# Optimization experiments

Hardware: AMD Instinct MI355X
Metric: run time of the kernel (lower is better)

## Reference

```python
import jax, jax.numpy as jnp
import numpy as np

N_NODES = 50000
N_EDGES = 800000
HEADS = 6
LEAKY = 0.2


def gat_layer(x, W, a_src, a_dst, src, dst):
    """Multi-head GAT layer (Velickovic et al.), concat heads + ELU.
    x: [N, F_in], W: [H, F_in, F_out], a_src/a_dst: [H, F_out]."""
    n = x.shape[0]
    h = jnp.einsum('nf,hfo->nho', x, W)              # [N, H, F_out]
    es = jnp.einsum('nho,ho->nh', h, a_src)          # source attention term
    ed = jnp.einsum('nho,ho->nh', h, a_dst)          # destination attention term
    e = jax.nn.leaky_relu(es[src] + ed[dst], LEAKY)  # [E, H] per-edge logits
    # segment softmax over incoming edges of each destination node
    emax = jax.ops.segment_max(e, dst, num_segments=n)
    emax = jnp.where(jnp.isfinite(emax), emax, jnp.zeros_like(emax))
    ex = jnp.exp(e - emax[dst])                      # [E, H]
    denom = jax.ops.segment_sum(ex, dst, num_segments=n)
    alpha = ex / (denom[dst] + 1e-16)                # [E, H]
    msg = alpha[:, :, None] * h[src]                 # [E, H, F_out]
    out = jax.ops.segment_sum(msg, dst, num_segments=n)  # [N, H, F_out]
    return jax.nn.elu(out).reshape(n, -1)            # concat heads


def setup_inputs() -> dict:
    key = jax.random.key(0)
    ks = jax.random.split(key, 16)
    glorot = lambda k, shape: jax.random.normal(k, shape, jnp.float32) * np.sqrt(2.0 / (shape[-2] + shape[-1]))
    inp = {
        'x': jax.random.normal(ks[0], (N_NODES, 11), jnp.float32),
        'edge_index': jax.random.randint(ks[1], (2, N_EDGES), 0, N_NODES, jnp.int32),
        'W1': glorot(ks[2], (HEADS, 11, 16)),
        'a1s': glorot(ks[3], (HEADS, 16)),
        'a1d': glorot(ks[4], (HEADS, 16)),
        'W2': glorot(ks[5], (HEADS, 96, 32)),
        'a2s': glorot(ks[6], (HEADS, 32)),
        'a2d': glorot(ks[7], (HEADS, 32)),
        'W3': glorot(ks[8], (HEADS, 192, 64)),
        'a3s': glorot(ks[9], (HEADS, 64)),
        'a3d': glorot(ks[10], (HEADS, 64)),
        'Wd': glorot(ks[11], (384, 1)),
        'bd': jnp.zeros((1,), jnp.float32),
    }
    return inp


def reference(x, edge_index, W1, a1s, a1d, W2, a2s, a2d, W3, a3s, a3d, Wd, bd):
    src, dst = edge_index[0], edge_index[1]
    h = gat_layer(x, W1, a1s, a1d, src, dst)   # [N, 96]
    h = gat_layer(h, W2, a2s, a2d, src, dst)   # [N, 192]
    h = gat_layer(h, W3, a3s, a3d, src, dst)   # [N, 384]
    g = jnp.sum(h, axis=0).reshape(1, -1)      # sum pool -> [1, 384]
    g = g / jnp.maximum(jnp.linalg.norm(g, axis=1, keepdims=True), 1e-12)  # F.normalize
    out = g @ Wd + bd                          # Dense 384->1, linear nonlin
    return jnp.squeeze(out, 1)                 # [1]
```

## Files before the change

### kernel.cpp

```cpp
#include <hip/hip_runtime.h>
#include <hip/hip_bf16.h>


#define HHEADS 6

typedef __attribute__((ext_vector_type(8))) short bf16x8;
typedef __attribute__((ext_vector_type(4))) float f32x4;
typedef __attribute__((ext_vector_type(2))) float f32x2;

typedef __attribute__((address_space(3))) unsigned int lds_uint;
typedef const __attribute__((address_space(1))) unsigned int glb_uint;

__device__ __forceinline__ float bfl(unsigned u) { return __uint_as_float(u << 16); }
__device__ __forceinline__ float bfh(unsigned u) { return __uint_as_float(u & 0xffff0000u); }
__device__ __forceinline__ unsigned short f2bf(float v) {
    unsigned u = __float_as_uint(v);
    return (unsigned short)((u + 0x7fffu + ((u >> 16) & 1u)) >> 16);
}
__device__ __forceinline__ float bf2f(unsigned short h) {
    return __uint_as_float((unsigned)h << 16);
}
__device__ __forceinline__ unsigned fkey(float f) {
    unsigned u = __float_as_uint(f);
    return (u >> 31) ? ~u : (u | 0x80000000u);
}
__device__ __forceinline__ float funkey(unsigned k) {
    return (k >> 31) ? __uint_as_float(k & 0x7fffffffu) : __uint_as_float(~k);
}

__device__ __forceinline__ void xpose4(float& v0, float& v1, float& v2, float& v3, int b) {
    bool hi = (b & 2) != 0;
    float s0 = hi ? v0 : v2;
    float s1 = hi ? v1 : v3;
    s0 = __shfl_xor(s0, 2, 64);
    s1 = __shfl_xor(s1, 2, 64);
    v0 = hi ? s0 : v0;
    v1 = hi ? s1 : v1;
    v2 = hi ? v2 : s0;
    v3 = hi ? v3 : s1;
    bool od = (b & 1) != 0;
    float t0 = od ? v0 : v1;
    t0 = __shfl_xor(t0, 1, 64);
    v0 = od ? t0 : v0;
    v1 = od ? v1 : t0;
    float t1 = od ? v2 : v3;
    t1 = __shfl_xor(t1, 1, 64);
    v2 = od ? t1 : v2;
    v3 = od ? v3 : t1;
}

__global__ void zero_misc(int* __restrict__ count, int* __restrict__ cursor,
                          float* __restrict__ g, unsigned* __restrict__ gmax,
                          unsigned short* __restrict__ apH,
                          long pad3_off, long pad3_cnt, long pad6_off, long pad6_cnt, int n) {
    long i = (long)blockIdx.x * blockDim.x + threadIdx.x;
    long stride = (long)gridDim.x * blockDim.x;
    for (long j = i; j < n; j += stride) {
        count[j] = 0;
        cursor[j] = 0;
    }
    if (i < 384) g[i] = 0.f;
    if (i < 12) gmax[i] = 0u;
    for (long j = i; j < pad3_cnt; j += stride) apH[pad3_off + j] = 0;
    for (long j = i; j < pad6_cnt; j += stride) apH[pad6_off + j] = 0;
}

__global__ void hist_kernel(const int* __restrict__ dst, int* __restrict__ count, int E) {
    int e = blockIdx.x * blockDim.x + threadIdx.x;
    if (e >= E) return;
    atomicAdd(&count[dst[e]], 1);
}

__global__ void scan_block(const int* __restrict__ count, int* __restrict__ offsets,
                           int* __restrict__ bsum, int n) {
    __shared__ int s[1024];
    int i = blockIdx.x * 1024 + threadIdx.x;
    int v = (i < n) ? count[i] : 0;
    s[threadIdx.x] = v;
    __syncthreads();
    for (int off = 1; off < 1024; off <<= 1) {
        int t = (threadIdx.x >= (unsigned)off) ? s[threadIdx.x - off] : 0;
        __syncthreads();
        s[threadIdx.x] += t;
        __syncthreads();
    }
    if (i < n) offsets[i] = s[threadIdx.x] - v;
    if (threadIdx.x == 1023) bsum[blockIdx.x] = s[1023];
}

__global__ void scan_tops(int* __restrict__ bsum, int nb) {
    __shared__ int s[64];
    int t = threadIdx.x;
    int v = (t < nb) ? bsum[t] : 0;
    s[t] = v;
    __syncthreads();
    for (int off = 1; off < 64; off <<= 1) {
        int tmp = (t >= off) ? s[t - off] : 0;
        __syncthreads();
        s[t] += tmp;
        __syncthreads();
    }
    if (t < nb) bsum[t] = s[t] - v;
}

__global__ void scan_add(int* __restrict__ offsets, const int* __restrict__ bsum, int n,
                         int total) {
    int i = blockIdx.x * 1024 + threadIdx.x;
    if (i < n) offsets[i] += bsum[blockIdx.x];
    if (i == 0) offsets[n] = total;
}

__global__ void scatter_kernel(const int* __restrict__ src, const int* __restrict__ dst,
                               const int* __restrict__ offsets, int* __restrict__ cursor,
                               int* __restrict__ ssrc, int E) {
    int e = blockIdx.x * blockDim.x + threadIdx.x;
    if (e >= E) return;
    int d = dst[e];
    int pos = offsets[d] + atomicAdd(&cursor[d], 1);
    ssrc[pos] = src[e];
}

__global__ void repack_w(const float* __restrict__ W, float* __restrict__ Wp, int FIN, int F) {
    int HF = HHEADS * F;
    int i = blockIdx.x * blockDim.x + threadIdx.x;
    if (i >= FIN * HF) return;
    int k = i / HF, c = i % HF;
    int hd = c / F, f = c % F;
    Wp[i] = W[(hd * FIN + k) * F + f];
}

__global__ void repack_w_mfma(const float* __restrict__ W, unsigned short* __restrict__ bh,
                              int FIN, int F, int NPAD) {
    int i = blockIdx.x * blockDim.x + threadIdx.x;
    if (i >= FIN * NPAD) return;
    int k = i / NPAD, n = i % NPAD;
    int NKT = FIN / 32;
    int HF = HHEADS * F;
    float w = 0.f;
    if (n < HF) {
        int hd = n / F, f = n % F;
        w = W[(hd * FIN + k) * F + f];
    }
    size_t e = ((size_t)((n >> 4) * NKT + (k >> 5)) * 64 + ((n & 15) | (((k >> 3) & 3) << 4))) * 8 +
               (k & 7);
    bh[e] = f2bf(w);
}

template <int BM, int BN, int BK>
__global__ __launch_bounds__(256) void gemm_small_attn(const float* __restrict__ A,
                                                       const float* __restrict__ B,
                                                       unsigned char* __restrict__ C8,
                                                       const float* __restrict__ as_,
                                                       const float* __restrict__ ad_,
                                                       float* __restrict__ es,
                                                       float* __restrict__ ed, int M, int K,
                                                       int N) {
    __shared__ float As[BK][BM + 4];
    __shared__ float Bs[BK][BN];
    int tid = threadIdx.x;
    int tx = tid % 16, ty = tid / 16;
    int m0 = blockIdx.y * BM, n0 = blockIdx.x * BN;
    float acc[4][4] = {};
    for (int kk0 = 0; kk0 < K; kk0 += BK) {
#pragma unroll
        for (int i = 0; i < (BM * BK) / 256; ++i) {
            int idx = tid + i * 256;
            int m = idx / BK, k = idx % BK;
            float v = 0.f;
            if (m0 + m < M && kk0 + k < K) v = A[(size_t)(m0 + m) * K + kk0 + k];
            As[k][m] = v;
        }
#pragma unroll
        for (int i = 0; i < (BK * BN) / 1024; ++i) {
            int idx = tid + i * 256;
            int k = idx / (BN / 4), n4 = idx % (BN / 4);
            float4 v = make_float4(0.f, 0.f, 0.f, 0.f);
            if (kk0 + k < K && n0 + n4 * 4 < N)
                v = *(const float4*)&B[(size_t)(kk0 + k) * N + n0 + n4 * 4];
            *(float4*)&Bs[k][n4 * 4] = v;
        }
        __syncthreads();
#pragma unroll
        for (int k = 0; k < BK; ++k) {
            float4 av = *(const float4*)&As[k][ty * 4];
            float4 bv = *(const float4*)&Bs[k][tx * 4];
            float a[4] = {av.x, av.y, av.z, av.w};
            float b[4] = {bv.x, bv.y, bv.z, bv.w};
#pragma unroll
            for (int i = 0; i < 4; ++i)
#pragma unroll
                for (int j = 0; j < 4; ++j) acc[i][j] += a[i] * b[j];
        }
        __syncthreads();
    }
    bool colok = (n0 + tx * 4) < N;
    float asv[4], adv[4];
#pragma unroll
    for (int j = 0; j < 4; ++j) {
        int col = n0 + tx * 4 + j;
        asv[j] = (col < N) ? as_[col] : 0.f;
        adv[j] = (col < N) ? ad_[col] : 0.f;
    }
#pragma unroll
    for (int i = 0; i < 4; ++i) {
        int m = m0 + ty * 4 + i;
        bool mok = m < M;
        if (mok && colok) {
            int pk = __builtin_amdgcn_cvt_pk_fp8_f32(acc[i][0], acc[i][1], 0, false);
            pk = __builtin_amdgcn_cvt_pk_fp8_f32(acc[i][2], acc[i][3], pk, true);
            *(unsigned*)&C8[(size_t)m * N + n0 + tx * 4] = (unsigned)pk;
        }
        float ps = 0.f, pd = 0.f;
#pragma unroll
        for (int j = 0; j < 4; ++j) {
            ps += acc[i][j] * asv[j];
            pd += acc[i][j] * adv[j];
        }
        ps += __shfl_down(ps, 2, 4);
        ps += __shfl_down(ps, 1, 4);
        pd += __shfl_down(pd, 2, 4);
        pd += __shfl_down(pd, 1, 4);
        if (mok && colok && (tx & 3) == 0) {
            int hd = (n0 + tx * 4) >> 4;
            es[(size_t)m * HHEADS + hd] = ps;
            ed[(size_t)m * HHEADS + hd] = pd;
        }
    }
}

template <int K, int NREAL, int NPAD, int F, int MT>
__global__ __launch_bounds__(256) void gemm_attn_mfma(
    const unsigned short* __restrict__ Ah, const unsigned short* __restrict__ Bh,
    unsigned char* __restrict__ C8, const float* __restrict__ as_,
    const float* __restrict__ ad_, float* __restrict__ es, float* __restrict__ ed,
    unsigned* __restrict__ gmax, int M) {
    constexpr int NKT = K / 32;
    __shared__ unsigned short sB[NKT * 4096];
    __shared__ unsigned short sA[2][4096];
    int tid = threadIdx.x;
    int lane = tid & 63, wave = tid >> 6;
    int wrow = wave >> 1, wcol = wave & 1;
    int quad = lane >> 4, c16 = lane & 15;

    int nwg = gridDim.x * gridDim.y;
    int hh = blockIdx.y * gridDim.x + blockIdx.x;
    int q = nwg >> 3, r = nwg & 7;
    int xcd = hh & 7, pos = hh >> 3;
    int wk = (xcd < r ? xcd * (q + 1) : r * (q + 1) + (xcd - r) * q) + pos;
    int bx = wk % gridDim.x, by = wk / gridDim.x;

    int n0 = bx * 128;
    int bn16 = n0 >> 4;
    int nmt = (M + 127) >> 7;

#pragma unroll
    for (int kt2 = 0; kt2 < NKT; ++kt2) {
#pragma unroll
        for (int rep = 0; rep < 2; ++rep) {
            int chunk = tid + rep * 256;
            int tile = chunk >> 6, e8 = chunk & 63;
            size_t boff = ((size_t)((bn16 + tile) * NKT + kt2) * 64 + e8) * 8;
            __builtin_amdgcn_global_load_lds((glb_uint*)&Bh[boff],
                                             (lds_uint*)&sB[kt2 * 4096 + chunk * 8], 16, 0, 0);
        }
    }
    auto STAGE_A = [&](int mti, int kt2, int buf) {
#pragma unroll
        for (int rep = 0; rep < 2; ++rep) {
            int chunk = tid + rep * 256;
            int tile = chunk >> 6, e8 = chunk & 63;
            size_t aoff = ((size_t)((mti * 8 + tile) * NKT + kt2) * 64 + e8) * 8;
            __builtin_amdgcn_global_load_lds((glb_uint*)&Ah[aoff],
                                             (lds_uint*)&sA[buf][chunk * 8], 16, 0, 0);
        }
    };
    STAGE_A(min(by * MT, nmt - 1), 0, 0);
    asm volatile("s_waitcnt vmcnt(0)" ::: "memory");
    __builtin_amdgcn_s_barrier();

    float asv[4], adv[4];
#pragma unroll
    for (int j = 0; j < 4; ++j) {
        int col = n0 + wcol * 64 + j * 16 + c16;
        bool ok = col < NREAL;
        asv[j] = ok ? as_[col] : 0.f;
        adv[j] = ok ? ad_[col] : 0.f;
    }
    float mx = -1e30f;
    float mxA = -1e30f, mxB = -1e30f;
    bool colvalid = (n0 + wcol * 64) < NREAL;
    int b4 = lane & 3;

    f32x4 acc[4][4] = {};
    const int T = MT * NKT;
    int mt = 0, kt = 0;
    for (int t = 0; t < T; ++t) {
        int cur = t & 1;
        int nkt = kt + 1, nmt2 = mt;
        if (nkt == NKT) {
            nkt = 0;
            nmt2 = mt + 1;
        }
        if (t + 1 < T) STAGE_A(min(by * MT + nmt2, nmt - 1), nkt, cur ^ 1);
        bf16x8 fah[4], fbh[4];
#pragma unroll
        for (int i = 0; i < 4; ++i) {
            fah[i] = *(const bf16x8*)&sA[cur][(wrow * 4 + i) * 512 + lane * 8];
            fbh[i] = *(const bf16x8*)&sB[kt * 4096 + (wcol * 4 + i) * 512 + lane * 8];
        }
        asm volatile("s_waitcnt lgkmcnt(0)" ::: "memory");
        __builtin_amdgcn_sched_barrier(0);
#pragma unroll
        for (int i = 0; i < 4; ++i)
#pragma unroll
            for (int j = 0; j < 4; ++j)
                acc[i][j] = __builtin_amdgcn_mfma_f32_16x16x32_bf16(fah[i], fbh[j], acc[i][j],
                                                                    0, 0, 0);
        if (kt == NKT - 1) {
            int m0 = (by * MT + mt) * 128;
            if (m0 < M) {
#pragma unroll
                for (int i = 0; i < 4; ++i) {
#pragma unroll
                    for (int r2 = 0; r2 < 4; ++r2) {
                        int m = m0 + wrow * 64 + i * 16 + quad * 4 + r2;
                        bool mok = m < M;
                        if (F == 64) {
                            float ps = acc[i][0][r2] * asv[0] + acc[i][1][r2] * asv[1] +
                                       acc[i][2][r2] * asv[2] + acc[i][3][r2] * asv[3];
                            float pd = acc[i][0][r2] * adv[0] + acc[i][1][r2] * adv[1] +
                                       acc[i][2][r2] * adv[2] + acc[i][3][r2] * adv[3];
#pragma unroll
                            for (int off = 8; off > 0; off >>= 1) {
                                ps += __shfl_down(ps, off, 16);
                                pd += __shfl_down(pd, off, 16);
                            }
                            if (mok && c16 == 0) {
                                int hd = (n0 + wcol * 64) / 64;
                                es[(size_t)m * HHEADS + hd] = ps;
                                ed[(size_t)m * HHEADS + hd] = pd;
                                mx = fmaxf(mx, ps);
                            }
                        } else {
                            float psA = acc[i][0][r2] * asv[0] + acc[i][1][r2] * asv[1];
                            float pdA = acc[i][0][r2] * adv[0] + acc[i][1][r2] * adv[1];
                            float psB = acc[i][2][r2] * asv[2] + acc[i][3][r2] * asv[3];
                            float pdB = acc[i][2][r2] * adv[2] + acc[i][3][r2] * adv[3];
#pragma unroll
                            for (int off = 8; off > 0; off >>= 1) {
                                psA += __shfl_down(psA, off, 16);
                                pdA += __shfl_down(pdA, off, 16);
                                psB += __shfl_down(psB, off, 16);
                                pdB += __shfl_down(pdB, off, 16);
                            }
                            if (mok && c16 == 0 && colvalid) {
                                int colbase = n0 + wcol * 64;
                                int hd = colbase / 32;
                                es[(size_t)m * HHEADS + hd] = psA;
                                ed[(size_t)m * HHEADS + hd] = pdA;
                                es[(size_t)m * HHEADS + hd + 1] = psB;
                                ed[(size_t)m * HHEADS + hd + 1] = pdB;
                                mxA = fmaxf(mxA, psA);
                                mxB = fmaxf(mxB, psB);
                            }
                        }
                    }
                }
#pragma unroll
                for (int i = 0; i < 4; ++i) {
                    int m = m0 + wrow * 64 + i * 16 + quad * 4 + b4;
                    bool mok = m < M;
#pragma unroll
                    for (int j = 0; j < 4; ++j) {
                        float v0 = acc[i][j][0], v1 = acc[i][j][1], v2 = acc[i][j][2],
                              v3 = acc[i][j][3];
                        xpose4(v0, v1, v2, v3, b4);
                        int colb = n0 + wcol * 64 + j * 16 + (c16 & 12);
                        if (mok && (F == 64 || colvalid)) {
                            int pk = __builtin_amdgcn_cvt_pk_fp8_f32(v0, v1, 0, false);
                            pk = __builtin_amdgcn_cvt_pk_fp8_f32(v2, v3, pk, true);
                            *(unsigned*)&C8[(size_t)m * NREAL + colb] = (unsigned)pk;
                        }
                    }
                }
            }
#pragma unroll
            for (int i = 0; i < 4; ++i)
#pragma unroll
                for (int j = 0; j < 4; ++j) acc[i][j] = (f32x4){0.f, 0.f, 0.f, 0.f};
        }
        asm volatile("s_waitcnt vmcnt(0)" ::: "memory");
        __builtin_amdgcn_s_barrier();
        kt = nkt;
        mt = nmt2;
    }

    if (F == 64) {
#pragma unroll
        for (int off = 32; off > 0; off >>= 1) mx = fmaxf(mx, __shfl_xor(mx, off));
        if (lane == 0) atomicMax(&gmax[(n0 + wcol * 64) / 64], fkey(mx));
    } else {
        mxA = fmaxf(mxA, __shfl_xor(mxA, 16));
        mxA = fmaxf(mxA, __shfl_xor(mxA, 32));
        mxB = fmaxf(mxB, __shfl_xor(mxB, 16));
        mxB = fmaxf(mxB, __shfl_xor(mxB, 32));
        if (lane == 0 && colvalid) {
            int hd = (n0 + wcol * 64) / 32;
            atomicMax(&gmax[6 + hd], fkey(mxA));
            atomicMax(&gmax[6 + hd + 1], fkey(mxB));
        }
    }
}

template <int F>
__global__ __launch_bounds__(256) void aggregate_fused(
    const unsigned char* __restrict__ h8, const float* __restrict__ es,
    const float* __restrict__ ed, const int* __restrict__ offsets,
    const int* __restrict__ ssrc, unsigned short* __restrict__ oh, int n) {
    constexpr int HF = HHEADS * F;
    constexpr int C8 = HF / 8;
    int tid = blockIdx.x * blockDim.x + threadIdx.x;
    if (tid >= n * C8) return;
    int node = tid / C8, q = tid % C8;
    int c = q * 8, hd = c / F;
    int a = offsets[node], b = offsets[node + 1];
    float edv = ed[node * HHEADS + hd];
    float m = -1e30f, l = 0.f;
    f32x2 a0 = {0.f, 0.f}, a1 = {0.f, 0.f}, a2 = {0.f, 0.f}, a3 = {0.f, 0.f};
    for (int j = a; j < b; ++j) {
        int s = ssrc[j];
        float v = es[s * HHEADS + hd] + edv;
        v = v > 0.f ? v : 0.2f * v;
        float mn = fmaxf(m, v);
        float r = __expf(m - mn);
        float wgt = __expf(v - mn);
        uint2 hv = *(const uint2*)&h8[(size_t)s * HF + c];
        f32x2 p0 = __builtin_amdgcn_cvt_pk_f32_fp8((int)hv.x, false);
        f32x2 p1 = __builtin_amdgcn_cvt_pk_f32_fp8((int)hv.x, true);
        f32x2 p2 = __builtin_amdgcn_cvt_pk_f32_fp8((int)hv.y, false);
        f32x2 p3 = __builtin_amdgcn_cvt_pk_f32_fp8((int)hv.y, true);
        l = l * r + wgt;
        f32x2 rv = {r, r}, wv = {wgt, wgt};
        a0 = a0 * rv + wv * p0;
        a1 = a1 * rv + wv * p1;
        a2 = a2 * rv + wv * p2;
        a3 = a3 * rv + wv * p3;
        m = mn;
    }
    float invd = 1.0f / (l + 1e-16f);
    float res[8] = {a0[0], a0[1], a1[0], a1[1], a2[0], a2[1], a3[0], a3[1]};
    unsigned short th[8];
#pragma unroll
    for (int k = 0; k < 8; ++k) {
        float v = res[k] * invd;
        v = v > 0.f ? v : (__expf(v) - 1.0f);
        th[k] = f2bf(v);
    }
    constexpr int NKT = HF / 32;
    int lq = (node & 15) | (((c >> 3) & 3) << 4);
    size_t base = ((size_t)((node >> 4) * NKT + (c >> 5)) * 64 + lq) * 8;
    *(uint4*)&oh[base] = *(uint4*)th;
}

__global__ __launch_bounds__(256) void aggregate_wpn2(
    const unsigned char* __restrict__ h8, const float* __restrict__ es,
    const float* __restrict__ ed, const unsigned* __restrict__ gmax,
    const int* __restrict__ offsets, const int* __restrict__ ssrc,
    unsigned short* __restrict__ oh, int n) {
    constexpr int HF = 192;
    int wid = (int)((blockIdx.x * (unsigned)blockDim.x + threadIdx.x) >> 6);
    int lane = threadIdx.x & 63;
    if (wid >= n || lane >= 48) return;
    int node = wid;
    int hd = lane >> 3;
    int c = lane * 4;
    int a = offsets[node], b = offsets[node + 1];
    float edv = ed[node * HHEADS + hd];
    float mv = funkey(gmax[6 + hd]) + edv;
    float m = mv > 0.f ? mv : 0.2f * mv;
    float l = 0.f;
    f32x2 a0 = {0.f, 0.f}, a1 = {0.f, 0.f};
    const unsigned char* hbase = h8 + c;
    int j = a;
    for (; j + 3 < b; j += 4) {
        int s0 = ssrc[j], s1 = ssrc[j + 1], s2 = ssrc[j + 2], s3 = ssrc[j + 3];
        float ev0 = es[(size_t)s0 * HHEADS + hd];
        float ev1 = es[(size_t)s1 * HHEADS + hd];
        float ev2 = es[(size_t)s2 * HHEADS + hd];
        float ev3 = es[(size_t)s3 * HHEADS + hd];
        unsigned h0 = *(const unsigned*)(hbase + (size_t)s0 * HF);
        unsigned h1 = *(const unsigned*)(hbase + (size_t)s1 * HF);
        unsigned h2 = *(const unsigned*)(hbase + (size_t)s2 * HF);
        unsigned h3 = *(const unsigned*)(hbase + (size_t)s3 * HF);
        float v0 = ev0 + edv;
        v0 = v0 > 0.f ? v0 : 0.2f * v0;
        float v1 = ev1 + edv;
        v1 = v1 > 0.f ? v1 : 0.2f * v1;
        float v2 = ev2 + edv;
        v2 = v2 > 0.f ? v2 : 0.2f * v2;
        float v3 = ev3 + edv;
        v3 = v3 > 0.f ? v3 : 0.2f * v3;
        float w0 = __expf(v0 - m);
        float w1 = __expf(v1 - m);
        float w2 = __expf(v2 - m);
        float w3 = __expf(v3 - m);
        {
            f32x2 p0 = __builtin_amdgcn_cvt_pk_f32_fp8((int)h0, false);
            f32x2 p1 = __builtin_amdgcn_cvt_pk_f32_fp8((int)h0, true);
            f32x2 wv = {w0, w0};
            l += w0;
            a0 = a0 + wv * p0;
            a1 = a1 + wv * p1;
        }
        {
            f32x2 p0 = __builtin_amdgcn_cvt_pk_f32_fp8((int)h1, false);
            f32x2 p1 = __builtin_amdgcn_cvt_pk_f32_fp8((int)h1, true);
            f32x2 wv = {w1, w1};
            l += w1;
            a0 = a0 + wv * p0;
            a1 = a1 + wv * p1;
        }
        {
            f32x2 p0 = __builtin_amdgcn_cvt_pk_f32_fp8((int)h2, false);
            f32x2 p1 = __builtin_amdgcn_cvt_pk_f32_fp8((int)h2, true);
            f32x2 wv = {w2, w2};
            l += w2;
            a0 = a0 + wv * p0;
            a1 = a1 + wv * p1;
        }
        {
            f32x2 p0 = __builtin_amdgcn_cvt_pk_f32_fp8((int)h3, false);
            f32x2 p1 = __builtin_amdgcn_cvt_pk_f32_fp8((int)h3, true);
            f32x2 wv = {w3, w3};
            l += w3;
            a0 = a0 + wv * p0;
            a1 = a1 + wv * p1;
        }
    }
    for (; j < b; ++j) {
        int s0 = ssrc[j];
        float ev0 = es[(size_t)s0 * HHEADS + hd];
        unsigned h0 = *(const unsigned*)(hbase + (size_t)s0 * HF);
        float v0 = ev0 + edv;
        v0 = v0 > 0.f ? v0 : 0.2f * v0;
        float w0 = __expf(v0 - m);
        f32x2 p0 = __builtin_amdgcn_cvt_pk_f32_fp8((int)h0, false);
        f32x2 p1 = __builtin_amdgcn_cvt_pk_f32_fp8((int)h0, true);
        f32x2 wv = {w0, w0};
        l += w0;
        a0 = a0 + wv * p0;
        a1 = a1 + wv * p1;
    }
    float invd = 1.0f / (l + 1e-16f);
    float res[4] = {a0[0], a0[1], a1[0], a1[1]};
    unsigned short th[4];
#pragma unroll
    for (int k = 0; k < 4; ++k) {
        float v = res[k] * invd;
        v = v > 0.f ? v : (__expf(v) - 1.0f);
        th[k] = f2bf(v);
    }
    int lq = (node & 15) | (((c >> 3) & 3) << 4);
    size_t base = ((size_t)((node >> 4) * (HF / 32) + (c >> 5)) * 64 + lq) * 8 + (c & 7);
    *(uint2*)&oh[base] = *(uint2*)th;
}

__global__ __launch_bounds__(256) void aggregate_wpn3(
    const unsigned char* __restrict__ h8, const float* __restrict__ es,
    const float* __restrict__ ed, const unsigned* __restrict__ gmax,
    const int* __restrict__ offsets, const int* __restrict__ ssrc,
    __hip_bfloat16* __restrict__ outb, int n) {
    constexpr int HF = 384;
    int wid = (int)((blockIdx.x * (unsigned)blockDim.x + threadIdx.x) >> 6);
    int lane = threadIdx.x & 63;
    if (wid >= n || lane >= 48) return;
    int node = wid;
    int hd = lane >> 3;
    int c = lane * 8;
    int a = offsets[node], b = offsets[node + 1];
    float edv = ed[node * HHEADS + hd];
    float mv = funkey(gmax[hd]) + edv;
    float m = mv > 0.f ? mv : 0.2f * mv;
    float l = 0.f;
    f32x2 a0 = {0.f, 0.f}, a1 = {0.f, 0.f}, a2 = {0.f, 0.f}, a3 = {0.f, 0.f};
    const unsigned char* hbase = h8 + c;
    int j = a;
    for (; j + 3 < b; j += 4) {
        int s0 = ssrc[j], s1 = ssrc[j + 1], s2 = ssrc[j + 2], s3 = ssrc[j + 3];
        float ev0 = es[(size_t)s0 * HHEADS + hd];
        float ev1 = es[(size_t)s1 * HHEADS + hd];
        float ev2 = es[(size_t)s2 * HHEADS + hd];
        float ev3 = es[(size_t)s3 * HHEADS + hd];
        uint2 h0 = *(const uint2*)(hbase + (size_t)s0 * HF);
        uint2 h1 = *(const uint2*)(hbase + (size_t)s1 * HF);
        uint2 h2 = *(const uint2*)(hbase + (size_t)s2 * HF);
        uint2 h3 = *(const uint2*)(hbase + (size_t)s3 * HF);
        float v0 = ev0 + edv;
        v0 = v0 > 0.f ? v0 : 0.2f * v0;
        float v1 = ev1 + edv;
        v1 = v1 > 0.f ? v1 : 0.2f * v1;
        float v2 = ev2 + edv;
        v2 = v2 > 0.f ? v2 : 0.2f * v2;
        float v3 = ev3 + edv;
        v3 = v3 > 0.f ? v3 : 0.2f * v3;
        float w0 = __expf(v0 - m);
        float w1 = __expf(v1 - m);
        float w2 = __expf(v2 - m);
        float w3 = __expf(v3 - m);
        {
            f32x2 p0 = __builtin_amdgcn_cvt_pk_f32_fp8((int)h0.x, false);
            f32x2 p1 = __builtin_amdgcn_cvt_pk_f32_fp8((int)h0.x, true);
            f32x2 p2 = __builtin_amdgcn_cvt_pk_f32_fp8((int)h0.y, false);
            f32x2 p3 = __builtin_amdgcn_cvt_pk_f32_fp8((int)h0.y, true);
            f32x2 wv = {w0, w0};
            l += w0;
            a0 = a0 + wv * p0;
            a1 = a1 + wv * p1;
            a2 = a2 + wv * p2;
            a3 = a3 + wv * p3;
        }
        {
            f32x2 p0 = __builtin_amdgcn_cvt_pk_f32_fp8((int)h1.x, false);
            f32x2 p1 = __builtin_amdgcn_cvt_pk_f32_fp8((int)h1.x, true);
            f32x2 p2 = __builtin_amdgcn_cvt_pk_f32_fp8((int)h1.y, false);
            f32x2 p3 = __builtin_amdgcn_cvt_pk_f32_fp8((int)h1.y, true);
            f32x2 wv = {w1, w1};
            l += w1;
            a0 = a0 + wv * p0;
            a1 = a1 + wv * p1;
            a2 = a2 + wv * p2;
            a3 = a3 + wv * p3;
        }
        {
            f32x2 p0 = __builtin_amdgcn_cvt_pk_f32_fp8((int)h2.x, false);
            f32x2 p1 = __builtin_amdgcn_cvt_pk_f32_fp8((int)h2.x, true);
            f32x2 p2 = __builtin_amdgcn_cvt_pk_f32_fp8((int)h2.y, false);
            f32x2 p3 = __builtin_amdgcn_cvt_pk_f32_fp8((int)h2.y, true);
            f32x2 wv = {w2, w2};
            l += w2;
            a0 = a0 + wv * p0;
            a1 = a1 + wv * p1;
            a2 = a2 + wv * p2;
            a3 = a3 + wv * p3;
        }
        {
            f32x2 p0 = __builtin_amdgcn_cvt_pk_f32_fp8((int)h3.x, false);
            f32x2 p1 = __builtin_amdgcn_cvt_pk_f32_fp8((int)h3.x, true);
            f32x2 p2 = __builtin_amdgcn_cvt_pk_f32_fp8((int)h3.y, false);
            f32x2 p3 = __builtin_amdgcn_cvt_pk_f32_fp8((int)h3.y, true);
            f32x2 wv = {w3, w3};
            l += w3;
            a0 = a0 + wv * p0;
            a1 = a1 + wv * p1;
            a2 = a2 + wv * p2;
            a3 = a3 + wv * p3;
        }
    }
    for (; j < b; ++j) {
        int s0 = ssrc[j];
        float ev0 = es[(size_t)s0 * HHEADS + hd];
        uint2 h0 = *(const uint2*)(hbase + (size_t)s0 * HF);
        float v0 = ev0 + edv;
        v0 = v0 > 0.f ? v0 : 0.2f * v0;
        float w0 = __expf(v0 - m);
        f32x2 p0 = __builtin_amdgcn_cvt_pk_f32_fp8((int)h0.x, false);
        f32x2 p1 = __builtin_amdgcn_cvt_pk_f32_fp8((int)h0.x, true);
        f32x2 p2 = __builtin_amdgcn_cvt_pk_f32_fp8((int)h0.y, false);
        f32x2 p3 = __builtin_amdgcn_cvt_pk_f32_fp8((int)h0.y, true);
        f32x2 wv = {w0, w0};
        l += w0;
        a0 = a0 + wv * p0;
        a1 = a1 + wv * p1;
        a2 = a2 + wv * p2;
        a3 = a3 + wv * p3;
    }
    float invd = 1.0f / (l + 1e-16f);
    float res[8] = {a0[0], a0[1], a1[0], a1[1], a2[0], a2[1], a3[0], a3[1]};
    __hip_bfloat16 tb[8];
#pragma unroll
    for (int k = 0; k < 8; ++k) {
        float v = res[k] * invd;
        v = v > 0.f ? v : (__expf(v) - 1.0f);
        tb[k] = __float2bfloat16(v);
    }
    *(uint4*)&outb[(size_t)node * HF + c] = *(uint4*)tb;
}

__global__ void pool_kernel(const __hip_bfloat16* __restrict__ out3, float* __restrict__ g,
                            int n) {
    int b = blockIdx.x, t = threadIdx.x;
    int chunk = (n + gridDim.x - 1) / gridDim.x;
    int n0 = b * chunk, n1 = min(n, n0 + chunk);
    float a0 = 0.f, a1 = 0.f;
    const unsigned* p = (const unsigned*)out3;
    for (int node = n0; node < n1; ++node) {
        unsigned u = p[(size_t)node * 192 + t];
        a0 += bfl(u);
        a1 += bfh(u);
    }
    atomicAdd(&g[2 * t], a0);
    atomicAdd(&g[2 * t + 1], a1);
}

__global__ void final_kernel(const float* __restrict__ g, const float* __restrict__ Wd,
                             const float* __restrict__ bd, float* __restrict__ outp) {
    __shared__ float red[384];
    int t = threadIdx.x;
    float v = g[t];
    red[t] = v * v;
    __syncthreads();
    for (int s = 192; s >= 3; s >>= 1) {
        if (t < s) red[t] += red[t + s];
        __syncthreads();
    }
    __shared__ float scale_s;
    if (t == 0) {
        float norm = sqrtf(red[0] + red[1] + red[2]);
        scale_s = 1.0f / fmaxf(norm, 1e-12f);
    }
    __syncthreads();
    float scale = scale_s;
    red[t] = v * scale * Wd[t];
    __syncthreads();
    for (int s = 192; s >= 3; s >>= 1) {
        if (t < s) red[t] += red[t + s];
        __syncthreads();
    }
    if (t == 0) outp[0] = red[0] + red[1] + red[2] + bd[0];
}

extern "C" void kernel_launch(void* const* d_in, const int* in_sizes, int n_in, void* d_out,
                              int out_size, void* d_ws, size_t ws_size, hipStream_t stream) {
    const float* x = (const float*)d_in[0];
    const int* ei = (const int*)d_in[1];
    const float* W1 = (const float*)d_in[2];
    const float* a1s = (const float*)d_in[3];
    const float* a1d = (const float*)d_in[4];
    const float* W2 = (const float*)d_in[5];
    const float* a2s = (const float*)d_in[6];
    const float* a2d = (const float*)d_in[7];
    const float* W3 = (const float*)d_in[8];
    const float* a3s = (const float*)d_in[9];
    const float* a3d = (const float*)d_in[10];
    const float* Wd = (const float*)d_in[11];
    const float* bd = (const float*)d_in[12];
    float* outp = (float*)d_out;

    const int N = in_sizes[0] / 11;
    const int E = in_sizes[1] / 2;
    const int* src = ei;
    const int* dst = ei + E;

    const int NT16 = ((N + 127) / 128) * 8;
    const int NMT = (N + 127) / 128;

    char* w = (char*)d_ws;
    size_t off = 0;
    auto A = [&](size_t bytes) {
        size_t o = off;
        off += (bytes + 255) & ~(size_t)255;
        return o;
    };
    unsigned char* bufH = (unsigned char*)(w + A((size_t)N * 384 * 2));
    __hip_bfloat16* bufO = (__hip_bfloat16*)(w + A((size_t)N * 384 * 2));
    unsigned short* apH = (unsigned short*)(w + A((size_t)NT16 * 6 * 512 * 2));
    unsigned short* b2H = (unsigned short*)(w + A((size_t)16 * 3 * 512 * 2));
    unsigned short* b3H = (unsigned short*)(w + A((size_t)24 * 6 * 512 * 2));
    float* es = (float*)(w + A((size_t)N * HHEADS * 4));
    float* ed = (float*)(w + A((size_t)N * HHEADS * 4));
    unsigned* gmax = (unsigned*)(w + A(256));
    float* wp = (float*)(w + A((size_t)11 * 96 * 4));
    int* count = (int*)(w + A((size_t)(N + 1) * 4));
    int* cursor = (int*)(w + A((size_t)(N + 1) * 4));
    int* offsets = (int*)(w + A((size_t)(N + 1) * 4));
    int* bsum = (int*)(w + A(64 * 4));
    int* ssrc = (int*)(w + A((size_t)E * 4));
    float* g = (float*)(w + A(384 * 4));

    const long t16v = N / 16;
    const long padT = NT16 - t16v;
    zero_misc<<<(N + 255) / 256, 256, 0, stream>>>(count, cursor, g, gmax, apH,
                                                   t16v * 3 * 512, padT * 3 * 512,
                                                   t16v * 6 * 512, padT * 6 * 512, N);

    hist_kernel<<<(E + 255) / 256, 256, 0, stream>>>(dst, count, E);
    int nb = (N + 1023) / 1024;
    scan_block<<<nb, 1024, 0, stream>>>(count, offsets, bsum, N);
    scan_tops<<<1, 64, 0, stream>>>(bsum, nb);
    scan_add<<<nb, 1024, 0, stream>>>(offsets, bsum, N, E);
    scatter_kernel<<<(E + 255) / 256, 256, 0, stream>>>(src, dst, offsets, cursor, ssrc, E);

    repack_w<<<(11 * 96 + 255) / 256, 256, 0, stream>>>(W1, wp, 11, 16);
    repack_w_mfma<<<(96 * 256 + 255) / 256, 256, 0, stream>>>(W2, b2H, 96, 32, 256);
    repack_w_mfma<<<(192 * 384 + 255) / 256, 256, 0, stream>>>(W3, b3H, 192, 64, 384);

    {
        dim3 grid((96 + 63) / 64, (N + 63) / 64);
        gemm_small_attn<64, 64, 32><<<grid, 256, 0, stream>>>(x, wp, bufH, a1s, a1d, es, ed, N,
                                                              11, 96);
    }
    {
        long total = (long)N * (96 / 8);
        aggregate_fused<16><<<(total + 255) / 256, 256, 0, stream>>>(bufH, es, ed, offsets,
                                                                     ssrc, apH, N);
    }

    {
        dim3 grid(2, (NMT + 3) / 4);
        gemm_attn_mfma<96, 192, 256, 32, 4><<<grid, 256, 0, stream>>>(apH, b2H, bufH, a2s,
                                                                      a2d, es, ed, gmax, N);
    }
    {
        int grid = (N + 3) / 4;
        aggregate_wpn2<<<grid, 256, 0, stream>>>(bufH, es, ed, gmax, offsets, ssrc, apH, N);
    }

    {
        dim3 grid(3, (NMT + 3) / 4);
        gemm_attn_mfma<192, 384, 384, 64, 4><<<grid, 256, 0, stream>>>(apH, b3H, bufH, a3s,
                                                                       a3d, es, ed, gmax, N);
    }
    {
        int grid = (N + 3) / 4;
        aggregate_wpn3<<<grid, 256, 0, stream>>>(bufH, es, ed, gmax, offsets, ssrc, bufO, N);
    }

    pool_kernel<<<256, 192, 0, stream>>>(bufO, g, N);
    final_kernel<<<1, 384, 0, stream>>>(g, Wd, bd, outp);
}
```

Baseline: 489.3 us.

## Fuse sum-pooling into final GAT aggregation with replicated atomic partials

The layer-3 aggregation kernel now reduces its per-node ELU outputs within each block in shared memory and atomically adds them into 64 replicated partial-sum vectors, instead of writing a bf16 [N,384] tensor that a separate pool kernel reads back. The final kernel sums the 64 replicas before normalising. This removes a full write and read of the layer-3 output and one launch, at the cost of a block-wide barrier, per-block atomics, and a change in floating-point summation order.

```diff
diff --git a/kernel.cpp b/kernel.cpp
--- a/kernel.cpp
+++ b/kernel.cpp
@@ -50,7 +50,7 @@
 }
 
 __global__ void zero_misc(int* __restrict__ count, int* __restrict__ cursor,
-                          float* __restrict__ g, unsigned* __restrict__ gmax,
+                          float* __restrict__ gmid, unsigned* __restrict__ gmax,
                           unsigned short* __restrict__ apH,
                           long pad3_off, long pad3_cnt, long pad6_off, long pad6_cnt, int n) {
     long i = (long)blockIdx.x * blockDim.x + threadIdx.x;
@@ -59,7 +59,7 @@
         count[j] = 0;
         cursor[j] = 0;
     }
-    if (i < 384) g[i] = 0.f;
+    for (long j = i; j < 64 * 384; j += stride) gmid[j] = 0.f;
     if (i < 12) gmax[i] = 0u;
     for (long j = i; j < pad3_cnt; j += stride) apH[pad3_off + j] = 0;
     for (long j = i; j < pad6_cnt; j += stride) apH[pad6_off + j] = 0;
@@ -569,45 +569,103 @@
     const unsigned char* __restrict__ h8, const float* __restrict__ es,
     const float* __restrict__ ed, const unsigned* __restrict__ gmax,
     const int* __restrict__ offsets, const int* __restrict__ ssrc,
-    __hip_bfloat16* __restrict__ outb, int n) {
+    float* __restrict__ gmid, int n) {
     constexpr int HF = 384;
-    int wid = (int)((blockIdx.x * (unsigned)blockDim.x + threadIdx.x) >> 6);
-    int lane = threadIdx.x & 63;
-    if (wid >= n || lane >= 48) return;
+    __shared__ float gp[4][384];
+    int wave = threadIdx.x >> 6, lane = threadIdx.x & 63;
+    int wid = blockIdx.x * 4 + wave;
     int node = wid;
     int hd = lane >> 3;
     int c = lane * 8;
-    int a = offsets[node], b = offsets[node + 1];
-    float edv = ed[node * HHEADS + hd];
-    float mv = funkey(gmax[hd]) + edv;
-    float m = mv > 0.f ? mv : 0.2f * mv;
-    float l = 0.f;
-    f32x2 a0 = {0.f, 0.f}, a1 = {0.f, 0.f}, a2 = {0.f, 0.f}, a3 = {0.f, 0.f};
-    const unsigned char* hbase = h8 + c;
-    int j = a;
-    for (; j + 3 < b; j += 4) {
-        int s0 = ssrc[j], s1 = ssrc[j + 1], s2 = ssrc[j + 2], s3 = ssrc[j + 3];
-        float ev0 = es[(size_t)s0 * HHEADS + hd];
-        float ev1 = es[(size_t)s1 * HHEADS + hd];
-        float ev2 = es[(size_t)s2 * HHEADS + hd];
-        float ev3 = es[(size_t)s3 * HHEADS + hd];
-        uint2 h0 = *(const uint2*)(hbase + (size_t)s0 * HF);
-        uint2 h1 = *(const uint2*)(hbase + (size_t)s1 * HF);
-        uint2 h2 = *(const uint2*)(hbase + (size_t)s2 * HF);
-        uint2 h3 = *(const uint2*)(hbase + (size_t)s3 * HF);
-        float v0 = ev0 + edv;
-        v0 = v0 > 0.f ? v0 : 0.2f * v0;
-        float v1 = ev1 + edv;
-        v1 = v1 > 0.f ? v1 : 0.2f * v1;
-        float v2 = ev2 + edv;
-        v2 = v2 > 0.f ? v2 : 0.2f * v2;
-        float v3 = ev3 + edv;
-        v3 = v3 > 0.f ? v3 : 0.2f * v3;
-        float w0 = __expf(v0 - m);
-        float w1 = __expf(v1 - m);
-        float w2 = __expf(v2 - m);
-        float w3 = __expf(v3 - m);
-        {
+    bool active = (wid < n) && (lane < 48);
+    float res[8] = {};
+    if (active) {
+        int a = offsets[node], b = offsets[node + 1];
+        float edv = ed[node * HHEADS + hd];
+        float mv = funkey(gmax[hd]) + edv;
+        float m = mv > 0.f ? mv : 0.2f * mv;
+        float l = 0.f;
+        f32x2 a0 = {0.f, 0.f}, a1 = {0.f, 0.f}, a2 = {0.f, 0.f}, a3 = {0.f, 0.f};
+        const unsigned char* hbase = h8 + c;
+        int j = a;
+        for (; j + 3 < b; j += 4) {
+            int s0 = ssrc[j], s1 = ssrc[j + 1], s2 = ssrc[j + 2], s3 = ssrc[j + 3];
+            float ev0 = es[(size_t)s0 * HHEADS + hd];
+            float ev1 = es[(size_t)s1 * HHEADS + hd];
+            float ev2 = es[(size_t)s2 * HHEADS + hd];
+            float ev3 = es[(size_t)s3 * HHEADS + hd];
+            uint2 h0 = *(const uint2*)(hbase + (size_t)s0 * HF);
+            uint2 h1 = *(const uint2*)(hbase + (size_t)s1 * HF);
+            uint2 h2 = *(const uint2*)(hbase + (size_t)s2 * HF);
+            uint2 h3 = *(const uint2*)(hbase + (size_t)s3 * HF);
+            float v0 = ev0 + edv;
+            v0 = v0 > 0.f ? v0 : 0.2f * v0;
+            float v1 = ev1 + edv;
+            v1 = v1 > 0.f ? v1 : 0.2f * v1;
+            float v2 = ev2 + edv;
+            v2 = v2 > 0.f ? v2 : 0.2f * v2;
+            float v3 = ev3 + edv;
+            v3 = v3 > 0.f ? v3 : 0.2f * v3;
+            float w0 = __expf(v0 - m);
+            float w1 = __expf(v1 - m);
+            float w2 = __expf(v2 - m);
+            float w3 = __expf(v3 - m);
+            {
+                f32x2 p0 = __builtin_amdgcn_cvt_pk_f32_fp8((int)h0.x, false);
+                f32x2 p1 = __builtin_amdgcn_cvt_pk_f32_fp8((int)h0.x, true);
+                f32x2 p2 = __builtin_amdgcn_cvt_pk_f32_fp8((int)h0.y, false);
+                f32x2 p3 = __builtin_amdgcn_cvt_pk_f32_fp8((int)h0.y, true);
+                f32x2 wv = {w0, w0};
+                l += w0;
+                a0 = a0 + wv * p0;
+                a1 = a1 + wv * p1;
+                a2 = a2 + wv * p2;
+                a3 = a3 + wv * p3;
+            }
+            {
+                f32x2 p0 = __builtin_amdgcn_cvt_pk_f32_fp8((int)h1.x, false);
+                f32x2 p1 = __builtin_amdgcn_cvt_pk_f32_fp8((int)h1.x, true);
+                f32x2 p2 = __builtin_amdgcn_cvt_pk_f32_fp8((int)h1.y, false);
+                f32x2 p3 = __builtin_amdgcn_cvt_pk_f32_fp8((int)h1.y, true);
+                f32x2 wv = {w1, w1};
+                l += w1;
+                a0 = a0 + wv * p0;
+                a1 = a1 + wv * p1;
+                a2 = a2 + wv * p2;
+                a3 = a3 + wv * p3;
+            }
+            {
+                f32x2 p0 = __builtin_amdgcn_cvt_pk_f32_fp8((int)h2.x, false);
+                f32x2 p1 = __builtin_amdgcn_cvt_pk_f32_fp8((int)h2.x, true);
+                f32x2 p2 = __builtin_amdgcn_cvt_pk_f32_fp8((int)h2.y, false);
+                f32x2 p3 = __builtin_amdgcn_cvt_pk_f32_fp8((int)h2.y, true);
+                f32x2 wv = {w2, w2};
+                l += w2;
+                a0 = a0 + wv * p0;
+                a1 = a1 + wv * p1;
+                a2 = a2 + wv * p2;
+                a3 = a3 + wv * p3;
+            }
+            {
+                f32x2 p0 = __builtin_amdgcn_cvt_pk_f32_fp8((int)h3.x, false);
+                f32x2 p1 = __builtin_amdgcn_cvt_pk_f32_fp8((int)h3.x, true);
+                f32x2 p2 = __builtin_amdgcn_cvt_pk_f32_fp8((int)h3.y, false);
+                f32x2 p3 = __builtin_amdgcn_cvt_pk_f32_fp8((int)h3.y, true);
+                f32x2 wv = {w3, w3};
+                l += w3;
+                a0 = a0 + wv * p0;
+                a1 = a1 + wv * p1;
+                a2 = a2 + wv * p2;
+                a3 = a3 + wv * p3;
+            }
+        }
+        for (; j < b; ++j) {
+            int s0 = ssrc[j];
+            float ev0 = es[(size_t)s0 * HHEADS + hd];
+            uint2 h0 = *(const uint2*)(hbase + (size_t)s0 * HF);
+            float v0 = ev0 + edv;
+            v0 = v0 > 0.f ? v0 : 0.2f * v0;
+            float w0 = __expf(v0 - m);
             f32x2 p0 = __builtin_amdgcn_cvt_pk_f32_fp8((int)h0.x, false);
             f32x2 p1 = __builtin_amdgcn_cvt_pk_f32_fp8((int)h0.x, true);
             f32x2 p2 = __builtin_amdgcn_cvt_pk_f32_fp8((int)h0.y, false);
@@ -619,94 +677,32 @@
             a2 = a2 + wv * p2;
             a3 = a3 + wv * p3;
         }
-        {
-            f32x2 p0 = __builtin_amdgcn_cvt_pk_f32_fp8((int)h1.x, false);
-            f32x2 p1 = __builtin_amdgcn_cvt_pk_f32_fp8((int)h1.x, true);
-            f32x2 p2 = __builtin_amdgcn_cvt_pk_f32_fp8((int)h1.y, false);
-            f32x2 p3 = __builtin_amdgcn_cvt_pk_f32_fp8((int)h1.y, true);
-            f32x2 wv = {w1, w1};
-            l += w1;
-            a0 = a0 + wv * p0;
-            a1 = a1 + wv * p1;
-            a2 = a2 + wv * p2;
-            a3 = a3 + wv * p3;
-        }
-        {
-            f32x2 p0 = __builtin_amdgcn_cvt_pk_f32_fp8((int)h2.x, false);
-            f32x2 p1 = __builtin_amdgcn_cvt_pk_f32_fp8((int)h2.x, true);
-            f32x2 p2 = __builtin_amdgcn_cvt_pk_f32_fp8((int)h2.y, false);
-            f32x2 p3 = __builtin_amdgcn_cvt_pk_f32_fp8((int)h2.y, true);
-            f32x2 wv = {w2, w2};
-            l += w2;
-            a0 = a0 + wv * p0;
-            a1 = a1 + wv * p1;
-            a2 = a2 + wv * p2;
-            a3 = a3 + wv * p3;
-        }
-        {
-            f32x2 p0 = __builtin_amdgcn_cvt_pk_f32_fp8((int)h3.x, false);
-            f32x2 p1 = __builtin_amdgcn_cvt_pk_f32_fp8((int)h3.x, true);
-            f32x2 p2 = __builtin_amdgcn_cvt_pk_f32_fp8((int)h3.y, false);
-            f32x2 p3 = __builtin_amdgcn_cvt_pk_f32_fp8((int)h3.y, true);
-            f32x2 wv = {w3, w3};
-            l += w3;
-            a0 = a0 + wv * p0;
-            a1 = a1 + wv * p1;
-            a2 = a2 + wv * p2;
-            a3 = a3 + wv * p3;
-        }
-    }
-    for (; j < b; ++j) {
-        int s0 = ssrc[j];
-        float ev0 = es[(size_t)s0 * HHEADS + hd];
-        uint2 h0 = *(const uint2*)(hbase + (size_t)s0 * HF);
-        float v0 = ev0 + edv;
-        v0 = v0 > 0.f ? v0 : 0.2f * v0;
-        float w0 = __expf(v0 - m);
-        f32x2 p0 = __builtin_amdgcn_cvt_pk_f32_fp8((int)h0.x, false);
-        f32x2 p1 = __builtin_amdgcn_cvt_pk_f32_fp8((int)h0.x, true);
-        f32x2 p2 = __builtin_amdgcn_cvt_pk_f32_fp8((int)h0.y, false);
-        f32x2 p3 = __builtin_amdgcn_cvt_pk_f32_fp8((int)h0.y, true);
-        f32x2 wv = {w0, w0};
-        l += w0;
-        a0 = a0 + wv * p0;
-        a1 = a1 + wv * p1;
-        a2 = a2 + wv * p2;
-        a3 = a3 + wv * p3;
-    }
-    float invd = 1.0f / (l + 1e-16f);
-    float res[8] = {a0[0], a0[1], a1[0], a1[1], a2[0], a2[1], a3[0], a3[1]};
-    __hip_bfloat16 tb[8];
-#pragma unroll
-    for (int k = 0; k < 8; ++k) {
-        float v = res[k] * invd;
-        v = v > 0.f ? v : (__expf(v) - 1.0f);
-        tb[k] = __float2bfloat16(v);
-    }
-    *(uint4*)&outb[(size_t)node * HF + c] = *(uint4*)tb;
-}
-
-__global__ void pool_kernel(const __hip_bfloat16* __restrict__ out3, float* __restrict__ g,
-                            int n) {
-    int b = blockIdx.x, t = threadIdx.x;
-    int chunk = (n + gridDim.x - 1) / gridDim.x;
-    int n0 = b * chunk, n1 = min(n, n0 + chunk);
-    float a0 = 0.f, a1 = 0.f;
-    const unsigned* p = (const unsigned*)out3;
-    for (int node = n0; node < n1; ++node) {
-        unsigned u = p[(size_t)node * 192 + t];
-        a0 += bfl(u);
-        a1 += bfh(u);
-    }
-    atomicAdd(&g[2 * t], a0);
-    atomicAdd(&g[2 * t + 1], a1);
-}
-
-__global__ void final_kernel(const float* __restrict__ g, const float* __restrict__ Wd,
+        float invd = 1.0f / (l + 1e-16f);
+        float t[8] = {a0[0], a0[1], a1[0], a1[1], a2[0], a2[1], a3[0], a3[1]};
+#pragma unroll
+        for (int k = 0; k < 8; ++k) {
+            float v = t[k] * invd;
+            res[k] = v > 0.f ? v : (__expf(v) - 1.0f);
+        }
+    }
+    if (lane < 48) {
+#pragma unroll
+        for (int k = 0; k < 8; ++k) gp[wave][c + k] = res[k];
+    }
+    __syncthreads();
+    int rep = blockIdx.x & 63;
+    for (int i = threadIdx.x; i < 384; i += 256) {
+        float s = gp[0][i] + gp[1][i] + gp[2][i] + gp[3][i];
+        atomicAdd(&gmid[rep * 384 + i], s);
+    }
+}
+
+__global__ void final_kernel(const float* __restrict__ gmid, const float* __restrict__ Wd,
                              const float* __restrict__ bd, float* __restrict__ outp) {
     __shared__ float red[384];
     int t = threadIdx.x;
-    float v = g[t];
+    float v = 0.f;
+    for (int r = 0; r < 64; ++r) v += gmid[r * 384 + t];
     red[t] = v * v;
     __syncthreads();
     for (int s = 192; s >= 3; s >>= 1) {
@@ -762,7 +758,7 @@
         return o;
     };
     unsigned char* bufH = (unsigned char*)(w + A((size_t)N * 384 * 2));
-    __hip_bfloat16* bufO = (__hip_bfloat16*)(w + A((size_t)N * 384 * 2));
+    float* gmid = (float*)(w + A((size_t)N * 384 * 2));
     unsigned short* apH = (unsigned short*)(w + A((size_t)NT16 * 6 * 512 * 2));
     unsigned short* b2H = (unsigned short*)(w + A((size_t)16 * 3 * 512 * 2));
     unsigned short* b3H = (unsigned short*)(w + A((size_t)24 * 6 * 512 * 2));
@@ -775,11 +771,10 @@
     int* offsets = (int*)(w + A((size_t)(N + 1) * 4));
     int* bsum = (int*)(w + A(64 * 4));
     int* ssrc = (int*)(w + A((size_t)E * 4));
-    float* g = (float*)(w + A(384 * 4));
 
     const long t16v = N / 16;
     const long padT = NT16 - t16v;
-    zero_misc<<<(N + 255) / 256, 256, 0, stream>>>(count, cursor, g, gmax, apH,
+    zero_misc<<<(N + 255) / 256, 256, 0, stream>>>(count, cursor, gmid, gmax, apH,
                                                    t16v * 3 * 512, padT * 3 * 512,
                                                    t16v * 6 * 512, padT * 6 * 512, N);
 
@@ -822,9 +817,8 @@
     }
     {
         int grid = (N + 3) / 4;
-        aggregate_wpn3<<<grid, 256, 0, stream>>>(bufH, es, ed, gmax, offsets, ssrc, bufO, N);
-    }
-
-    pool_kernel<<<256, 192, 0, stream>>>(bufO, g, N);
-    final_kernel<<<1, 384, 0, stream>>>(g, Wd, bd, outp);
-}
+        aggregate_wpn3<<<grid, 256, 0, stream>>>(bufH, es, ed, gmax, offsets, ssrc, gmid, N);
+    }
+
+    final_kernel<<<1, 384, 0, stream>>>(gmid, Wd, bd, outp);
+}
```

Measured after the change: 432.5 us. 1.13x faster.
